# Performance work log

Hardware: AMD Instinct MI355X
Metric: run time of the kernel (lower is better)

Reference implementation:

```python
import jax, jax.numpy as jnp
import numpy as np

N_NODES = 50000
N_EDGES = 600000
D = 128  # input_nf = output_nf = hidden_nf
EDGE_IN = 2 * D + 1   # source, target, radial
NODE_IN = 2 * D       # x, agg


def _glorot(key, shape):
    fan_in, fan_out = shape[0], shape[1]
    lim = float(np.sqrt(6.0 / (fan_in + fan_out)))
    return jax.random.uniform(key, shape, jnp.float32, -lim, lim)


def setup_inputs() -> dict:
    key = jax.random.key(0)
    ks = jax.random.split(key, 16)
    h = jax.random.normal(ks[0], (N_NODES, D), jnp.float32)
    edge_index = jax.random.randint(ks[1], (2, N_EDGES), 0, N_NODES, jnp.int64 if jax.config.read('jax_enable_x64') else jnp.int32)
    coord = jax.random.uniform(ks[2], (N_NODES, 3), jnp.float32)
    l = jnp.array([10.0, 10.0, 10.0], jnp.float32)  # periodic box lengths (non-trainable buffer)
    return {
        'h': h, 'edge_index': edge_index, 'coord': coord, 'num_nodes': N_NODES, 'l': l,
        # edge_mlp: Linear(257,128) SiLU Linear(128,128) SiLU
        'We1': _glorot(ks[3], (EDGE_IN, D)), 'be1': jnp.zeros((D,), jnp.float32),
        'We2': _glorot(ks[4], (D, D)),       'be2': jnp.zeros((D,), jnp.float32),
        # node_mlp: Linear(256,128) SiLU Linear(128,128)
        'Wn1': _glorot(ks[5], (NODE_IN, D)), 'bn1': jnp.zeros((D,), jnp.float32),
        'Wn2': _glorot(ks[6], (D, D)),       'bn2': jnp.zeros((D,), jnp.float32),
        # coord_mlp: Linear(128,128) SiLU Linear(128,1, bias=False, xavier gain=0.001)
        'Wc1': _glorot(ks[7], (D, D)),       'bc1': jnp.zeros((D,), jnp.float32),
        'Wc2': _glorot(ks[8], (D, 1)) * 0.001,
    }


def reference(h, edge_index, coord, num_nodes, l,
              We1, be1, We2, be2, Wn1, bn1, Wn2, bn2, Wc1, bc1, Wc2):
    row, col = edge_index[0], edge_index[1]

    # coord2radial with periodic minimum-image wrap
    diff = coord[row] - coord[col]                       # [E, 3]
    diff = jnp.where(diff > 0.5 * l, diff - l, diff)
    diff = jnp.where(diff < -0.5 * l, diff + l, diff)
    radial = jnp.sum(diff * diff, axis=1, keepdims=True)  # [E, 1]

    # edge model: gather -> concat -> 2-layer SiLU MLP
    eh = jnp.concatenate([h[row], h[col], radial], axis=1)  # [E, 257]
    eh = jax.nn.silu(eh @ We1 + be1)
    edge_feat = jax.nn.silu(eh @ We2 + be2)                 # [E, 128]

    # coord model: trans/agg computed in the original but discarded (dead code);
    # only the periodic remainder of coord is returned.
    coord_out = jnp.remainder(coord, l)

    # node model: scatter-add edge features into nodes, then MLP + residual
    agg = jax.ops.segment_sum(edge_feat, row, num_segments=num_nodes)  # [N, 128]
    nh = jnp.concatenate([h, agg], axis=1)                              # [N, 256]
    nh = jax.nn.silu(nh @ Wn1 + bn1)
    h_out = h + (nh @ Wn2 + bn2)

    return h_out, coord_out, edge_feat
```

## Files before the change

### kernel.cpp

```cpp
#include <hip/hip_runtime.h>
#include <math.h>

#define D 128
#define SXS 264
#define SHS 132
#define SFS 132

typedef unsigned int u32;
typedef unsigned short u16;
typedef __attribute__((ext_vector_type(8))) short bf16x8;
typedef __attribute__((ext_vector_type(4))) float f32x4;
typedef __attribute__((ext_vector_type(2))) float f32x2;

__device__ __forceinline__ float bfl(u32 u) { return __uint_as_float(u << 16); }
__device__ __forceinline__ float bfh(u32 u) { return __uint_as_float(u & 0xFFFF0000u); }
__device__ __forceinline__ u16 f2bf(float f) {
    u32 u = __float_as_uint(f);
    return (u16)((u + 0x7FFFu + ((u >> 16) & 1u)) >> 16);
}
__device__ __forceinline__ u32 cvt_pk_bf16(float lo, float hi) {
    u32 r;
    asm("v_cvt_pk_bf16_f32 %0, %1, %2" : "=v"(r) : "v"(lo), "v"(hi));
    return r;
}
__device__ __forceinline__ u16 cvt1_bf16(float v) { return (u16)cvt_pk_bf16(v, v); }
__device__ __forceinline__ float silu_f(float x) {
    float e = __expf(-x);
    return x * __builtin_amdgcn_rcpf(1.0f + e);
}
__device__ __forceinline__ void atomic_pk_add_bf16(u16* addr, u32 pk) {
    asm volatile("global_atomic_pk_add_bf16 %0, %1, off sc1"
                 :: "v"(addr), "v"(pk) : "memory");
}

__global__ void coord_kernel(const float* __restrict__ coord,
                             const float* __restrict__ lbox,
                             float* __restrict__ out, int n3) {
    int i = blockIdx.x * 256 + threadIdx.x;
    if (i < n3) {
        float ld = lbox[i % 3];
        float c = coord[i];
        float r = fmodf(c, ld);
        if (r < 0.f) r += ld;
        out[i] = r;
    }
}

__global__ void prep_weights(const float* __restrict__ We1, const float* __restrict__ We2,
                             const float* __restrict__ Wn1, const float* __restrict__ Wn2,
                             u16* __restrict__ wt) {
    int i = blockIdx.x * 256 + threadIdx.x;
    if (i < 32768)        { int n = i >> 8, k = i & 255;              wt[i] = f2bf(We1[(size_t)k*D + n]); }
    else if (i < 49152)   { int j = i - 32768; int n = j >> 7, k = j & 127; wt[i] = f2bf(We2[(size_t)k*D + n]); }
    else if (i < 81920)   { int j = i - 49152; int n = j >> 8, k = j & 255; wt[i] = f2bf(Wn1[(size_t)k*D + n]); }
    else if (i < 98304)   { int j = i - 81920; int n = j >> 7, k = j & 127; wt[i] = f2bf(Wn2[(size_t)k*D + n]); }
}

__global__ void hist_kernel(const int* __restrict__ ei, int* __restrict__ cnt, int E) {
    int e = blockIdx.x * 256 + threadIdx.x;
    if (e < E) atomicAdd(&cnt[ei[e]], 1);
}

__global__ void scan1_kernel(const int* __restrict__ cnt, int* __restrict__ offs,
                             int* __restrict__ bsum, int n ) {
    __shared__ int s[256];
    int t = threadIdx.x, b = blockIdx.x;
    int base = b * 1024 + t * 4;
    int v[4];
    #pragma unroll
    for (int i = 0; i < 4; ++i) { int idx = base + i; v[i] = (idx < n - 1) ? cnt[idx] : 0; }
    int lsum = v[0] + v[1] + v[2] + v[3];
    s[t] = lsum; __syncthreads();
    #pragma unroll
    for (int off = 1; off < 256; off <<= 1) {
        int x = (t >= off) ? s[t - off] : 0; __syncthreads();
        s[t] += x; __syncthreads();
    }
    int run = s[t] - lsum;
    #pragma unroll
    for (int i = 0; i < 4; ++i) { int idx = base + i; if (idx < n) offs[idx] = run; run += v[i]; }
    if (t == 255) bsum[b] = s[255];
}

__global__ void scan2_kernel(int* __restrict__ bsum, int nb) {
    __shared__ int s[64];
    int t = threadIdx.x;
    int orig = (t < nb) ? bsum[t] : 0;
    s[t] = orig; __syncthreads();
    #pragma unroll
    for (int off = 1; off < 64; off <<= 1) {
        int x = (t >= off) ? s[t - off] : 0; __syncthreads();
        s[t] += x; __syncthreads();
    }
    if (t < nb) bsum[t] = s[t] - orig;
}

__global__ void scan3_kernel(int* __restrict__ offs, const int* __restrict__ bsum,
                             int* __restrict__ cursor, int n) {
    int i = blockIdx.x * 256 + threadIdx.x;
    if (i < n) {
        int v = offs[i] + bsum[i >> 10];
        offs[i] = v;
        if (i < n - 1) cursor[i] = v;
    }
}

__global__ void scatter_kernel(const int* __restrict__ ei, int* __restrict__ cursor,
                               int* __restrict__ perm, int4* __restrict__ edata, int E) {
    int e = blockIdx.x * 256 + threadIdx.x;
    if (e < E) {
        int r = ei[e];
        int c = ei[(size_t)E + e];
        int p = atomicAdd(&cursor[r], 1);
        if (edata) edata[p] = make_int4(e, r, c, 0);
        else perm[p] = e;
    }
}

__global__ __launch_bounds__(256, 4) void pq_kernel(
    const float* __restrict__ h, const u16* __restrict__ wt,
    const float* __restrict__ be1,
    u16* __restrict__ Pt, u16* __restrict__ Qt,
    int* __restrict__ cursor, int N,
    const float* __restrict__ coord, const float* __restrict__ lbox,
    float* __restrict__ coord_out, int n3, int NBn)
{
    __shared__ __align__(16) u16 sA[64 * SHS];
    __shared__ __align__(16) u16 sO[64 * SHS];

    const int t = threadIdx.x;

    if (blockIdx.x >= NBn) {
        int i = (blockIdx.x - NBn) * 256 + t;
        if (i < n3) {
            float ld = lbox[i % 3];
            float c = coord[i];
            float r = fmodf(c, ld);
            if (r < 0.f) r += ld;
            coord_out[i] = r;
        }
        return;
    }

    const int lane = t & 63;
    const int wid = t >> 6;
    const int n0 = blockIdx.x * 64;

    if (t < 64) { int zi = n0 + t; if (zi < N) cursor[zi] = 0; }

    {
        const int e = t & 63, q = t >> 6;
        int ng = n0 + e; int ns = (ng < N) ? ng : N - 1;
        const float4* src = (const float4*)(h + (size_t)ns * D + q * 32);
        u16* dst = sA + e * SHS + q * 32;
        #pragma unroll
        for (int c = 0; c < 4; ++c) {
            float4 a = src[2 * c], b = src[2 * c + 1];
            *(uint4*)(dst + c * 8) = make_uint4(cvt_pk_bf16(a.x, a.y), cvt_pk_bf16(a.z, a.w),
                                               cvt_pk_bf16(b.x, b.y), cvt_pk_bf16(b.z, b.w));
        }
    }
    __syncthreads();

    const int lrow = lane & 15;
    const int kg = lane >> 4;
    const int g4 = kg * 4;
    const int nbase = wid * 32;

    f32x4 accP[4][2] = {}, accQ[4][2] = {};
    {
        bf16x8 Bt[8], Bm[8];
        #pragma unroll
        for (int nn = 0; nn < 2; ++nn)
            #pragma unroll
            for (int s = 0; s < 4; ++s) {
                const u16* bp = wt + (size_t)(nbase + nn * 16 + lrow) * 256 + s * 32 + kg * 8;
                Bt[nn * 4 + s] = *(const bf16x8*)bp;
                Bm[nn * 4 + s] = *(const bf16x8*)(bp + 128);
            }
        #pragma unroll
        for (int s = 0; s < 4; ++s) {
            bf16x8 a[4];
            #pragma unroll
            for (int m = 0; m < 4; ++m)
                a[m] = *(const bf16x8*)(sA + (m * 16 + lrow) * SHS + s * 32 + kg * 8);
            #pragma unroll
            for (int m = 0; m < 4; ++m)
                #pragma unroll
                for (int nn = 0; nn < 2; ++nn) {
                    accP[m][nn] = __builtin_amdgcn_mfma_f32_16x16x32_bf16(a[m], Bt[nn * 4 + s], accP[m][nn], 0, 0, 0);
                    accQ[m][nn] = __builtin_amdgcn_mfma_f32_16x16x32_bf16(a[m], Bm[nn * 4 + s], accQ[m][nn], 0, 0, 0);
                }
        }
    }

    #pragma unroll
    for (int nn = 0; nn < 2; ++nn) {
        int outc = nbase + nn * 16 + lrow;
        float bb = be1[outc];
        #pragma unroll
        for (int m = 0; m < 4; ++m)
            #pragma unroll
            for (int r = 0; r < 4; ++r)
                sO[(m * 16 + g4 + r) * SHS + outc] = cvt1_bf16(accP[m][nn][r] + bb);
    }
    __syncthreads();
    {
        const int f4 = t & 15, rb = t >> 4;
        #pragma unroll
        for (int p = 0; p < 4; ++p) {
            int row = rb + p * 16;
            int ng = n0 + row;
            if (ng < N)
                *(uint4*)(Pt + (size_t)ng * D + f4 * 8) = *(const uint4*)(sO + row * SHS + f4 * 8);
        }
    }
    __syncthreads();
    #pragma unroll
    for (int nn = 0; nn < 2; ++nn) {
        int outc = nbase + nn * 16 + lrow;
        #pragma unroll
        for (int m = 0; m < 4; ++m)
            #pragma unroll
            for (int r = 0; r < 4; ++r)
                sO[(m * 16 + g4 + r) * SHS + outc] = cvt1_bf16(accQ[m][nn][r]);
    }
    __syncthreads();
    {
        const int f4 = t & 15, rb = t >> 4;
        #pragma unroll
        for (int p = 0; p < 4; ++p) {
            int row = rb + p * 16;
            int ng = n0 + row;
            if (ng < N)
                *(uint4*)(Qt + (size_t)ng * D + f4 * 8) = *(const uint4*)(sO + row * SHS + f4 * 8);
        }
    }
}

__global__ __launch_bounds__(256, 8) void edge_pq_kernel(
    const u16* __restrict__ Pt, const u16* __restrict__ Qt,
    const int* __restrict__ ei, const int* __restrict__ perm,
    const int4* __restrict__ edata,
    const float* __restrict__ coord, const float* __restrict__ lbox,
    const u16* __restrict__ wt, const float* __restrict__ We1,
    const float* __restrict__ be2,
    float* __restrict__ ef_out, float* __restrict__ aggf,
    u16* __restrict__ agg16, int E)
{
    __shared__ __align__(16) u16 uni[64 * SHS];
    __shared__ int srow[64], scol[64], sEid[64];
    __shared__ float sRad[64];
    __shared__ float sW[128];
    u16* sH1 = uni;
    u16* sE16 = uni;

    const int t = threadIdx.x;
    const int lane = t & 63;
    const int wid = t >> 6;

    int p0;
    {
        const int nwg = gridDim.x;
        const int orig = blockIdx.x;
        const int q = nwg >> 3, r = nwg & 7;
        const int xcd = orig & 7, idx = orig >> 3;
        const int tile = (xcd < r ? xcd * (q + 1) : r * (q + 1) + (xcd - r) * q) + idx;
        p0 = tile * 64;
    }

    if (t < 64) {
        int slot = p0 + t;
        bool valid = slot < E;
        int cs = valid ? slot : (E - 1);
        int eg, rr, cc;
        if (edata) {
            int4 ed = edata[cs];
            eg = ed.x; rr = ed.y; cc = ed.z;
        } else {
            eg = perm[cs];
            rr = ei[eg];
            cc = ei[(size_t)E + eg];
        }
        sEid[t] = valid ? eg : -1;
        srow[t] = rr;
        scol[t] = cc;
        float rad = 0.f;
        #pragma unroll
        for (int d3 = 0; d3 < 3; ++d3) {
            float df = coord[(size_t)rr * 3 + d3] - coord[(size_t)cc * 3 + d3];
            float ld = lbox[d3];
            df = (df >  0.5f * ld) ? df - ld : df;
            df = (df < -0.5f * ld) ? df + ld : df;
            rad += df * df;
        }
        sRad[t] = rad;
    } else if (t < 192) {
        sW[t - 64] = We1[(size_t)256 * D + (t - 64)];
    }
    __syncthreads();

    {
        const int e = t & 63, q = t >> 6;
        const u16* Pp = Pt + (size_t)srow[e] * D;
        const u16* Qp = Qt + (size_t)scol[e] * D;
        const float rad = sRad[e];
        #pragma unroll
        for (int c0 = 0; c0 < 4; ++c0) {
            int j0 = q * 32 + c0 * 8;
            uint4 pu = *(const uint4*)(Pp + j0);
            uint4 qu = *(const uint4*)(Qp + j0);
            u32 pa[4] = {pu.x, pu.y, pu.z, pu.w};
            u32 qa[4] = {qu.x, qu.y, qu.z, qu.w};
            u32 ow[4];
            #pragma unroll
            for (int k = 0; k < 4; ++k) {
                float w0 = sW[j0 + 2 * k], w1 = sW[j0 + 2 * k + 1];
                float v0 = silu_f(bfl(pa[k]) + bfl(qa[k]) + rad * w0);
                float v1 = silu_f(bfh(pa[k]) + bfh(qa[k]) + rad * w1);
                ow[k] = cvt_pk_bf16(v0, v1);
            }
            *(uint4*)(sH1 + e * SHS + j0) = make_uint4(ow[0], ow[1], ow[2], ow[3]);
        }
    }
    __syncthreads();

    const int lrow = lane & 15;
    const int kg = lane >> 4;
    const int g4 = kg * 4;
    const int nbase = wid * 32;

    f32x4 acc2[4][2] = {};
    {
        bf16x8 B2[8];
        #pragma unroll
        for (int nn = 0; nn < 2; ++nn)
            #pragma unroll
            for (int s = 0; s < 4; ++s)
                B2[nn * 4 + s] = *(const bf16x8*)(wt + 32768 + (size_t)(nbase + nn * 16 + lrow) * 128 + s * 32 + kg * 8);
        #pragma unroll
        for (int s = 0; s < 4; ++s) {
            bf16x8 a[4];
            #pragma unroll
            for (int m = 0; m < 4; ++m)
                a[m] = *(const bf16x8*)(sH1 + (m * 16 + lrow) * SHS + s * 32 + kg * 8);
            #pragma unroll
            for (int m = 0; m < 4; ++m)
                #pragma unroll
                for (int nn = 0; nn < 2; ++nn)
                    acc2[m][nn] = __builtin_amdgcn_mfma_f32_16x16x32_bf16(a[m], B2[nn * 4 + s], acc2[m][nn], 0, 0, 0);
        }
    }
    __syncthreads();

    #pragma unroll
    for (int nn = 0; nn < 2; ++nn) {
        int outc = nbase + nn * 16 + lrow;
        float bb = be2[outc];
        #pragma unroll
        for (int m = 0; m < 4; ++m)
            #pragma unroll
            for (int r = 0; r < 4; ++r)
                sE16[(m * 16 + g4 + r) * SHS + outc] = cvt1_bf16(silu_f(acc2[m][nn][r] + bb));
    }
    __syncthreads();

    if (agg16) {
        const int cp = t & 63;
        const int g = t >> 6;
        const int ebeg = g * 16, eend = ebeg + 16;
        float r0 = 0.f, r1 = 0.f;
        int prev = srow[ebeg];
        for (int e = ebeg; e < eend; ++e) {
            int r = srow[e];
            if (r != prev) {
                if (r0 != 0.f || r1 != 0.f)
                    atomic_pk_add_bf16(agg16 + (size_t)prev * D + 2 * cp, cvt_pk_bf16(r0, r1));
                r0 = 0.f; r1 = 0.f; prev = r;
            }
            int eg = sEid[e];
            if (eg >= 0) {
                u32 pk2 = *(const u32*)(sE16 + e * SHS + 2 * cp);
                float v0 = bfl(pk2), v1 = bfh(pk2);
                f32x2 vv = {v0, v1};
                __builtin_nontemporal_store(vv, (f32x2*)&ef_out[(size_t)eg * D + 2 * cp]);
                r0 += v0; r1 += v1;
            }
        }
        if (r0 != 0.f || r1 != 0.f)
            atomic_pk_add_bf16(agg16 + (size_t)prev * D + 2 * cp, cvt_pk_bf16(r0, r1));
    } else {
        const int ct = t & 127;
        const int half = t >> 7;
        const int ebeg = half * 32, eend = ebeg + 32;
        float run = 0.f;
        int prev = srow[ebeg];
        for (int e = ebeg; e < eend; ++e) {
            int r = srow[e];
            if (r != prev) {
                if (run != 0.f) atomicAdd(&aggf[(size_t)prev * D + ct], run);
                run = 0.f; prev = r;
            }
            int eg = sEid[e];
            if (eg >= 0) {
                float v = __uint_as_float((u32)sE16[e * SHS + ct] << 16);
                __builtin_nontemporal_store(v, &ef_out[(size_t)eg * D + ct]);
                run += v;
            }
        }
        if (run != 0.f) atomicAdd(&aggf[(size_t)prev * D + ct], run);
    }
}

__global__ __launch_bounds__(256, 3) void edge_fb_kernel(
    const float* __restrict__ h,
    const int* __restrict__ ei, const int* __restrict__ perm,
    const float* __restrict__ coord, const float* __restrict__ lbox,
    const u16* __restrict__ wt,
    const float* __restrict__ We1, const float* __restrict__ be1,
    const float* __restrict__ be2,
    float* __restrict__ ef_out, float* __restrict__ aggf, int E)
{
    __shared__ __align__(16) u16 sX[64 * SXS];
    __shared__ __align__(16) u16 sH1[64 * SHS];
    __shared__ int srow[64], scol[64], sEid[64];
    __shared__ float sRad[64];

    const int t = threadIdx.x;
    const int lane = t & 63;
    const int wid = t >> 6;

    int p0;
    {
        const int nwg = gridDim.x;
        const int orig = blockIdx.x;
        const int q = nwg >> 3, r = nwg & 7;
        const int xcd = orig & 7, idx = orig >> 3;
        const int tile = (xcd < r ? xcd * (q + 1) : r * (q + 1) + (xcd - r) * q) + idx;
        p0 = tile * 64;
    }

    if (t < 64) {
        int slot = p0 + t;
        int eg = perm[(slot < E) ? slot : (E - 1)];
        sEid[t] = (p0 + t < E) ? eg : -1;
        srow[t] = ei[eg];
        scol[t] = ei[(size_t)E + eg];
    }
    __syncthreads();

    {
        const int e = t & 63;
        const int q = t >> 6;
        const int r = srow[e], c = scol[e];
        const float4* src = (const float4*)((q < 2) ? (h + (size_t)r * D + (q & 1) * 64)
                                                    : (h + (size_t)c * D + (q & 1) * 64));
        u16* dst = sX + e * SXS + q * 64;
        #pragma unroll
        for (int i = 0; i < 8; ++i) {
            float4 a = src[2 * i], b = src[2 * i + 1];
            *(uint4*)(dst + i * 8) = make_uint4(cvt_pk_bf16(a.x, a.y), cvt_pk_bf16(a.z, a.w),
                                               cvt_pk_bf16(b.x, b.y), cvt_pk_bf16(b.z, b.w));
        }
        if (t < 64) {
            int rr = srow[t], cc = scol[t];
            float rad = 0.f;
            #pragma unroll
            for (int d3 = 0; d3 < 3; ++d3) {
                float df = coord[(size_t)rr * 3 + d3] - coord[(size_t)cc * 3 + d3];
                float ld = lbox[d3];
                df = (df >  0.5f * ld) ? df - ld : df;
                df = (df < -0.5f * ld) ? df + ld : df;
                rad += df * df;
            }
            sRad[t] = rad;
        }
    }
    __syncthreads();

    const int lrow = lane & 15;
    const int kg = lane >> 4;
    const int g4 = kg * 4;
    const int nbase = wid * 32;

    f32x4 acc[4][2] = {};
    {
        bf16x8 B1[16];
        #pragma unroll
        for (int nn = 0; nn < 2; ++nn)
            #pragma unroll
            for (int s = 0; s < 8; ++s)
                B1[nn * 8 + s] = *(const bf16x8*)(wt + (size_t)(nbase + nn * 16 + lrow) * 256 + s * 32 + kg * 8);
        #pragma unroll
        for (int s = 0; s < 8; ++s) {
            bf16x8 a[4];
            #pragma unroll
            for (int m = 0; m < 4; ++m)
                a[m] = *(const bf16x8*)(sX + (m * 16 + lrow) * SXS + s * 32 + kg * 8);
            #pragma unroll
            for (int m = 0; m < 4; ++m)
                #pragma unroll
                for (int nn = 0; nn < 2; ++nn)
                    acc[m][nn] = __builtin_amdgcn_mfma_f32_16x16x32_bf16(a[m], B1[nn * 8 + s], acc[m][nn], 0, 0, 0);
        }
    }

    #pragma unroll
    for (int nn = 0; nn < 2; ++nn) {
        int outc = nbase + nn * 16 + lrow;
        float wl = We1[(size_t)256 * D + outc];
        float bb = be1[outc];
        #pragma unroll
        for (int m = 0; m < 4; ++m)
            #pragma unroll
            for (int r = 0; r < 4; ++r) {
                int e = m * 16 + g4 + r;
                float v = acc[m][nn][r] + sRad[e] * wl + bb;
                sH1[e * SHS + outc] = cvt1_bf16(silu_f(v));
            }
    }
    __syncthreads();

    f32x4 acc2[4][2] = {};
    {
        bf16x8 B2[8];
        #pragma unroll
        for (int nn = 0; nn < 2; ++nn)
            #pragma unroll
            for (int s = 0; s < 4; ++s)
                B2[nn * 4 + s] = *(const bf16x8*)(wt + 32768 + (size_t)(nbase + nn * 16 + lrow) * 128 + s * 32 + kg * 8);
        #pragma unroll
        for (int s = 0; s < 4; ++s) {
            bf16x8 a[4];
            #pragma unroll
            for (int m = 0; m < 4; ++m)
                a[m] = *(const bf16x8*)(sH1 + (m * 16 + lrow) * SHS + s * 32 + kg * 8);
            #pragma unroll
            for (int m = 0; m < 4; ++m)
                #pragma unroll
                for (int nn = 0; nn < 2; ++nn)
                    acc2[m][nn] = __builtin_amdgcn_mfma_f32_16x16x32_bf16(a[m], B2[nn * 4 + s], acc2[m][nn], 0, 0, 0);
        }
    }
    __syncthreads();

    float* sXf = (float*)sX;
    #pragma unroll
    for (int nn = 0; nn < 2; ++nn) {
        int outc = nbase + nn * 16 + lrow;
        float bb = be2[outc];
        #pragma unroll
        for (int m = 0; m < 4; ++m)
            #pragma unroll
            for (int r = 0; r < 4; ++r)
                sXf[(m * 16 + g4 + r) * SFS + outc] = silu_f(acc2[m][nn][r] + bb);
    }
    __syncthreads();

    {
        const int ct = t & 127;
        const int half = t >> 7;
        const int ebeg = half * 32, eend = ebeg + 32;
        float run = 0.f;
        int prev = srow[ebeg];
        for (int e = ebeg; e < eend; ++e) {
            int r = srow[e];
            if (r != prev) {
                if (run != 0.f) atomicAdd(&aggf[(size_t)prev * D + ct], run);
                run = 0.f; prev = r;
            }
            int eg = sEid[e];
            if (eg >= 0) {
                float v = sXf[e * SFS + ct];
                __builtin_nontemporal_store(v, &ef_out[(size_t)eg * D + ct]);
                run += v;
            }
        }
        if (run != 0.f) atomicAdd(&aggf[(size_t)prev * D + ct], run);
    }
}

__global__ __launch_bounds__(256, 4) void node_kernel(
    const float* __restrict__ h, const float* __restrict__ aggf,
    const u16* __restrict__ agg16,
    const u16* __restrict__ wt,
    const float* __restrict__ bn1, const float* __restrict__ bn2,
    float* __restrict__ h_out, int N)
{
    __shared__ __align__(16) u16 uni[64 * SXS];
    u16* sX = uni;
    u16* sH1 = uni;
    float* sXf = (float*)uni;

    const int t = threadIdx.x;
    const int lane = t & 63;
    const int wid = t >> 6;
    const int n0 = blockIdx.x * 64;

    {
        const int e = t & 63;
        const int q = t >> 6;
        int ng = n0 + e; int ns = (ng < N) ? ng : N - 1;
        u16* dst = sX + e * SXS + q * 64;
        if (q >= 2 && agg16) {
            const u16* src = agg16 + (size_t)ns * D + (q & 1) * 64;
            #pragma unroll
            for (int i = 0; i < 8; ++i)
                *(uint4*)(dst + i * 8) = *(const uint4*)(src + i * 8);
        } else {
            const float4* src = (const float4*)(((q < 2) ? h : aggf) + (size_t)ns * D + (q & 1) * 64);
            #pragma unroll
            for (int i = 0; i < 8; ++i) {
                float4 a = src[2 * i], b = src[2 * i + 1];
                *(uint4*)(dst + i * 8) = make_uint4(cvt_pk_bf16(a.x, a.y), cvt_pk_bf16(a.z, a.w),
                                                   cvt_pk_bf16(b.x, b.y), cvt_pk_bf16(b.z, b.w));
            }
        }
    }
    __syncthreads();

    const int lrow = lane & 15;
    const int kg = lane >> 4;
    const int g4 = kg * 4;
    const int nbase = wid * 32;

    f32x4 acc[4][2] = {};
    {
        bf16x8 B1[16];
        #pragma unroll
        for (int nn = 0; nn < 2; ++nn)
            #pragma unroll
            for (int s = 0; s < 8; ++s)
                B1[nn * 8 + s] = *(const bf16x8*)(wt + 49152 + (size_t)(nbase + nn * 16 + lrow) * 256 + s * 32 + kg * 8);
        #pragma unroll
        for (int s = 0; s < 8; ++s) {
            bf16x8 a[4];
            #pragma unroll
            for (int m = 0; m < 4; ++m)
                a[m] = *(const bf16x8*)(sX + (m * 16 + lrow) * SXS + s * 32 + kg * 8);
            #pragma unroll
            for (int m = 0; m < 4; ++m)
                #pragma unroll
                for (int nn = 0; nn < 2; ++nn)
                    acc[m][nn] = __builtin_amdgcn_mfma_f32_16x16x32_bf16(a[m], B1[nn * 8 + s], acc[m][nn], 0, 0, 0);
        }
    }
    __syncthreads();

    #pragma unroll
    for (int nn = 0; nn < 2; ++nn) {
        int outc = nbase + nn * 16 + lrow;
        float bb = bn1[outc];
        #pragma unroll
        for (int m = 0; m < 4; ++m)
            #pragma unroll
            for (int r = 0; r < 4; ++r)
                sH1[(m * 16 + g4 + r) * SHS + outc] = cvt1_bf16(silu_f(acc[m][nn][r] + bb));
    }
    __syncthreads();

    f32x4 acc2[4][2] = {};
    {
        bf16x8 B2[8];
        #pragma unroll
        for (int nn = 0; nn < 2; ++nn)
            #pragma unroll
            for (int s = 0; s < 4; ++s)
                B2[nn * 4 + s] = *(const bf16x8*)(wt + 81920 + (size_t)(nbase + nn * 16 + lrow) * 128 + s * 32 + kg * 8);
        #pragma unroll
        for (int s = 0; s < 4; ++s) {
            bf16x8 a[4];
            #pragma unroll
            for (int m = 0; m < 4; ++m)
                a[m] = *(const bf16x8*)(sH1 + (m * 16 + lrow) * SHS + s * 32 + kg * 8);
            #pragma unroll
            for (int m = 0; m < 4; ++m)
                #pragma unroll
                for (int nn = 0; nn < 2; ++nn)
                    acc2[m][nn] = __builtin_amdgcn_mfma_f32_16x16x32_bf16(a[m], B2[nn * 4 + s], acc2[m][nn], 0, 0, 0);
        }
    }
    __syncthreads();

    #pragma unroll
    for (int nn = 0; nn < 2; ++nn) {
        int outc = nbase + nn * 16 + lrow;
        float bb = bn2[outc];
        #pragma unroll
        for (int m = 0; m < 4; ++m)
            #pragma unroll
            for (int r = 0; r < 4; ++r)
                sXf[(m * 16 + g4 + r) * SFS + outc] = acc2[m][nn][r] + bb;
    }
    __syncthreads();

    {
        const int f4 = t & 31;
        const int nb = t >> 5;
        #pragma unroll
        for (int i = 0; i < 8; ++i) {
            int nl = nb + i * 8;
            int ng = n0 + nl;
            if (ng < N) {
                f32x4 v = *(const f32x4*)&sXf[nl * SFS + f4 * 4];
                const f32x4 hv = *(const f32x4*)&h[(size_t)ng * D + f4 * 4];
                v += hv;
                __builtin_nontemporal_store(v, (f32x4*)&h_out[(size_t)ng * D + f4 * 4]);
            }
        }
    }
}

extern "C" void kernel_launch(void* const* d_in, const int* in_sizes, int n_in,
                              void* d_out, int out_size, void* d_ws, size_t ws_size,
                              hipStream_t stream) {
    const float* h     = (const float*)d_in[0];
    const int*   ei    = (const int*)d_in[1];
    const float* coord = (const float*)d_in[2];
    const float* lbox  = (const float*)d_in[4];
    const float* We1   = (const float*)d_in[5];
    const float* be1   = (const float*)d_in[6];
    const float* We2   = (const float*)d_in[7];
    const float* be2   = (const float*)d_in[8];
    const float* Wn1   = (const float*)d_in[9];
    const float* bn1   = (const float*)d_in[10];
    const float* Wn2   = (const float*)d_in[11];
    const float* bn2   = (const float*)d_in[12];

    const int N = in_sizes[0] / D;
    const int E = in_sizes[1] / 2;

    float* out       = (float*)d_out;
    float* h_out     = out;
    float* coord_out = out + (size_t)N * D;
    float* ef_out    = coord_out + (size_t)N * 3;
    float* aggf      = h_out;

    int* wsi = (int*)d_ws;
    u16* wt     = (u16*)d_ws;
    int* offs   = wsi + 49152;
    int* cursor = offs + (N + 8);
    int* bsum   = cursor + (N + 8);
    int* perm   = bsum + 64;
    u16* Pt     = (u16*)(perm + E);
    u16* Qt     = Pt + (size_t)N * D;
    int4* edata = (int4*)(((uintptr_t)(Qt + (size_t)N * D) + 15) & ~(uintptr_t)15);
    u16* agg16  = (u16*)(edata + E);

    size_t need_pq  = (size_t)((char*)(Qt + (size_t)N * D) - (char*)d_ws);
    size_t need_ed  = (size_t)((char*)(edata + E) - (char*)d_ws);
    size_t need_a16 = (size_t)((char*)(agg16 + (size_t)N * D) - (char*)d_ws);
    const bool use_pq  = ws_size >= need_pq;
    const bool use_ed  = use_pq && ws_size >= need_ed;
    const bool use_a16 = use_ed && ws_size >= need_a16;
    int4* edp  = use_ed ? edata : nullptr;
    u16*  a16p = use_a16 ? agg16 : nullptr;

    const int nb1 = (N + 1 + 1023) / 1024;

    prep_weights<<<384, 256, 0, stream>>>(We1, We2, Wn1, Wn2, wt);
    if (use_pq) {
        const int NBn = (N + 63) / 64;
        const int NBc = (N * 3 + 255) / 256;
        pq_kernel<<<NBn + NBc, 256, 0, stream>>>(h, wt, be1, Pt, Qt, cursor, N,
                                                 coord, lbox, coord_out, N * 3, NBn);
    } else {
        hipMemsetAsync(cursor, 0, (size_t)N * sizeof(int), stream);
        coord_kernel<<<(N * 3 + 255) / 256, 256, 0, stream>>>(coord, lbox, coord_out, N * 3);
    }

    if (use_a16)
        hipMemsetAsync(agg16, 0, (size_t)N * D * sizeof(u16), stream);
    else
        hipMemsetAsync(aggf, 0, (size_t)N * D * sizeof(float), stream);

    hist_kernel<<<(E + 255) / 256, 256, 0, stream>>>(ei, cursor, E);
    scan1_kernel<<<nb1, 256, 0, stream>>>(cursor, offs, bsum, N + 1);
    scan2_kernel<<<1, 64, 0, stream>>>(bsum, nb1);
    scan3_kernel<<<(N + 1 + 255) / 256, 256, 0, stream>>>(offs, bsum, cursor, N + 1);
    scatter_kernel<<<(E + 255) / 256, 256, 0, stream>>>(ei, cursor, perm, edp, E);

    if (use_pq)
        edge_pq_kernel<<<(E + 63) / 64, 256, 0, stream>>>(
            Pt, Qt, ei, perm, edp, coord, lbox, wt, We1, be2, ef_out, aggf, a16p, E);
    else
        edge_fb_kernel<<<(E + 63) / 64, 256, 0, stream>>>(
            h, ei, perm, coord, lbox, wt, We1, be1, be2, ef_out, aggf, E);

    node_kernel<<<(N + 63) / 64, 256, 0, stream>>>(
        h, aggf, a16p, wt, bn1, bn2, h_out, N);
}
```

Before: 243.9 us.

## Merge setup launches, use single-pass decoupled scan, vectorize hist/scatter

```diff
diff --git a/kernel.cpp b/kernel.cpp
--- a/kernel.cpp
+++ b/kernel.cpp
@@ -46,23 +46,87 @@
     }
 }
 
-__global__ void prep_weights(const float* __restrict__ We1, const float* __restrict__ We2,
-                             const float* __restrict__ Wn1, const float* __restrict__ Wn2,
-                             u16* __restrict__ wt) {
-    int i = blockIdx.x * 256 + threadIdx.x;
-    if (i < 32768)        { int n = i >> 8, k = i & 255;              wt[i] = f2bf(We1[(size_t)k*D + n]); }
-    else if (i < 49152)   { int j = i - 32768; int n = j >> 7, k = j & 127; wt[i] = f2bf(We2[(size_t)k*D + n]); }
-    else if (i < 81920)   { int j = i - 49152; int n = j >> 8, k = j & 255; wt[i] = f2bf(Wn1[(size_t)k*D + n]); }
-    else if (i < 98304)   { int j = i - 81920; int n = j >> 7, k = j & 127; wt[i] = f2bf(Wn2[(size_t)k*D + n]); }
-}
-
-__global__ void hist_kernel(const int* __restrict__ ei, int* __restrict__ cnt, int E) {
-    int e = blockIdx.x * 256 + threadIdx.x;
-    if (e < E) atomicAdd(&cnt[ei[e]], 1);
+__global__ __launch_bounds__(256) void prep_plus_kernel(
+    const float* __restrict__ We1, const float* __restrict__ We2,
+    const float* __restrict__ Wn1, const float* __restrict__ Wn2,
+    u16* __restrict__ wt,
+    int* __restrict__ cursor, int N,
+    u16* __restrict__ agg16, long agg_n,
+    int* __restrict__ bstate,
+    int B1, int B2, int B3)
+{
+    const int b = blockIdx.x, t = threadIdx.x;
+    if (b < B1) {
+        int i = b * 256 + t;
+        if (i < 32768)        { int n = i >> 8, k = i & 255;              wt[i] = f2bf(We1[(size_t)k*D + n]); }
+        else if (i < 49152)   { int j = i - 32768; int n = j >> 7, k = j & 127; wt[i] = f2bf(We2[(size_t)k*D + n]); }
+        else if (i < 81920)   { int j = i - 49152; int n = j >> 8, k = j & 255; wt[i] = f2bf(Wn1[(size_t)k*D + n]); }
+        else                  { int j = i - 81920; int n = j >> 7, k = j & 127; wt[i] = f2bf(Wn2[(size_t)k*D + n]); }
+    } else if (b < B2) {
+        int i = ((b - B1) * 256 + t) * 4;
+        if (i + 3 < N) *(int4*)(cursor + i) = make_int4(0, 0, 0, 0);
+        else for (int k = 0; k < 4; ++k) if (i + k < N) cursor[i + k] = 0;
+    } else if (b < B3) {
+        long i = ((long)(b - B2) * 256 + t) * 8;
+        if (agg16 && i < agg_n) *(uint4*)(agg16 + i) = make_uint4(0, 0, 0, 0);
+    } else {
+        if (t < 64) bstate[t] = 0;
+    }
+}
+
+__global__ void hist4_kernel(const int* __restrict__ ei, int* __restrict__ cnt, int E) {
+    int i = (blockIdx.x * 256 + threadIdx.x) * 4;
+    if (i + 3 < E) {
+        int4 r = *(const int4*)(ei + i);
+        atomicAdd(&cnt[r.x], 1); atomicAdd(&cnt[r.y], 1);
+        atomicAdd(&cnt[r.z], 1); atomicAdd(&cnt[r.w], 1);
+    } else {
+        for (int k = 0; k < 4; ++k) if (i + k < E) atomicAdd(&cnt[ei[i + k]], 1);
+    }
+}
+
+__global__ __launch_bounds__(256) void scan_lb_kernel(int* __restrict__ cursor,
+                                                      int* __restrict__ bstate, int n) {
+    __shared__ int s[256];
+    __shared__ int sExcl;
+    const int t = threadIdx.x, b = blockIdx.x;
+    const int base = b * 1024 + t * 4;
+    int v[4];
+    #pragma unroll
+    for (int i = 0; i < 4; ++i) { int idx = base + i; v[i] = (idx < n - 1) ? cursor[idx] : 0; }
+    int lsum = v[0] + v[1] + v[2] + v[3];
+    s[t] = lsum; __syncthreads();
+    #pragma unroll
+    for (int off = 1; off < 256; off <<= 1) {
+        int x = (t >= off) ? s[t - off] : 0; __syncthreads();
+        s[t] += x; __syncthreads();
+    }
+    if (t == 0)
+        __hip_atomic_store(&bstate[b], 0x40000000 | s[255], __ATOMIC_RELEASE, __HIP_MEMORY_SCOPE_AGENT);
+    if (t < 64) {
+        int val = 0;
+        if (t < b) {
+            int st;
+            do { st = __hip_atomic_load(&bstate[t], __ATOMIC_ACQUIRE, __HIP_MEMORY_SCOPE_AGENT); }
+            while (!(st & 0x40000000));
+            val = st & 0x3FFFFFFF;
+        }
+        #pragma unroll
+        for (int off = 1; off < 64; off <<= 1) val += __shfl_xor(val, off, 64);
+        if (t == 0) sExcl = val;
+    }
+    __syncthreads();
+    int run = sExcl + s[t] - lsum;
+    #pragma unroll
+    for (int i = 0; i < 4; ++i) {
+        int idx = base + i;
+        if (idx < n - 1) cursor[idx] = run;
+        run += v[i];
+    }
 }
 
 __global__ void scan1_kernel(const int* __restrict__ cnt, int* __restrict__ offs,
-                             int* __restrict__ bsum, int n ) {
+                             int* __restrict__ bsum, int n) {
     __shared__ int s[256];
     int t = threadIdx.x, b = blockIdx.x;
     int base = b * 1024 + t * 4;
@@ -105,23 +169,41 @@
     }
 }
 
-__global__ void scatter_kernel(const int* __restrict__ ei, int* __restrict__ cursor,
-                               int* __restrict__ perm, int4* __restrict__ edata, int E) {
-    int e = blockIdx.x * 256 + threadIdx.x;
-    if (e < E) {
-        int r = ei[e];
-        int c = ei[(size_t)E + e];
-        int p = atomicAdd(&cursor[r], 1);
-        if (edata) edata[p] = make_int4(e, r, c, 0);
-        else perm[p] = e;
+__global__ void scatter4_kernel(const int* __restrict__ ei, int* __restrict__ cursor,
+                                int* __restrict__ perm, int4* __restrict__ edata, int E) {
+    int i = (blockIdx.x * 256 + threadIdx.x) * 4;
+    if (i + 3 < E) {
+        int4 r = *(const int4*)(ei + i);
+        int4 c = *(const int4*)(ei + (size_t)E + i);
+        int p0 = atomicAdd(&cursor[r.x], 1);
+        int p1 = atomicAdd(&cursor[r.y], 1);
+        int p2 = atomicAdd(&cursor[r.z], 1);
+        int p3 = atomicAdd(&cursor[r.w], 1);
+        if (edata) {
+            edata[p0] = make_int4(i,     r.x, c.x, 0);
+            edata[p1] = make_int4(i + 1, r.y, c.y, 0);
+            edata[p2] = make_int4(i + 2, r.z, c.z, 0);
+            edata[p3] = make_int4(i + 3, r.w, c.w, 0);
+        } else {
+            perm[p0] = i; perm[p1] = i + 1; perm[p2] = i + 2; perm[p3] = i + 3;
+        }
+    } else {
+        for (int k = 0; k < 4; ++k) {
+            int e = i + k;
+            if (e < E) {
+                int r = ei[e], c = ei[(size_t)E + e];
+                int p = atomicAdd(&cursor[r], 1);
+                if (edata) edata[p] = make_int4(e, r, c, 0);
+                else perm[p] = e;
+            }
+        }
     }
 }
 
 __global__ __launch_bounds__(256, 4) void pq_kernel(
     const float* __restrict__ h, const u16* __restrict__ wt,
     const float* __restrict__ be1,
-    u16* __restrict__ Pt, u16* __restrict__ Qt,
-    int* __restrict__ cursor, int N,
+    u16* __restrict__ Pt, u16* __restrict__ Qt, int N,
     const float* __restrict__ coord, const float* __restrict__ lbox,
     float* __restrict__ coord_out, int n3, int NBn)
 {
@@ -145,8 +227,6 @@
     const int lane = t & 63;
     const int wid = t >> 6;
     const int n0 = blockIdx.x * 64;
-
-    if (t < 64) { int zi = n0 + t; if (zi < N) cursor[zi] = 0; }
 
     {
         const int e = t & 63, q = t >> 6;
@@ -757,28 +837,37 @@
     u16*  a16p = use_a16 ? agg16 : nullptr;
 
     const int nb1 = (N + 1 + 1023) / 1024;
-
-    prep_weights<<<384, 256, 0, stream>>>(We1, We2, Wn1, Wn2, wt);
+    const bool lbscan = nb1 <= 64;
+
+    const long agg_n = (long)N * D;
+    const int B1 = 384;
+    const int B2 = B1 + (N / 4 + 255) / 256;
+    const int B3 = B2 + (use_a16 ? (int)((agg_n / 8 + 255) / 256) : 0);
+    const int Bt = B3 + 1;
+    prep_plus_kernel<<<Bt, 256, 0, stream>>>(We1, We2, Wn1, Wn2, wt,
+                                             cursor, N, a16p, agg_n, bsum, B1, B2, B3);
+
     if (use_pq) {
         const int NBn = (N + 63) / 64;
         const int NBc = (N * 3 + 255) / 256;
-        pq_kernel<<<NBn + NBc, 256, 0, stream>>>(h, wt, be1, Pt, Qt, cursor, N,
+        pq_kernel<<<NBn + NBc, 256, 0, stream>>>(h, wt, be1, Pt, Qt, N,
                                                  coord, lbox, coord_out, N * 3, NBn);
     } else {
-        hipMemsetAsync(cursor, 0, (size_t)N * sizeof(int), stream);
         coord_kernel<<<(N * 3 + 255) / 256, 256, 0, stream>>>(coord, lbox, coord_out, N * 3);
     }
 
-    if (use_a16)
-        hipMemsetAsync(agg16, 0, (size_t)N * D * sizeof(u16), stream);
-    else
+    if (!use_a16)
         hipMemsetAsync(aggf, 0, (size_t)N * D * sizeof(float), stream);
 
-    hist_kernel<<<(E + 255) / 256, 256, 0, stream>>>(ei, cursor, E);
-    scan1_kernel<<<nb1, 256, 0, stream>>>(cursor, offs, bsum, N + 1);
-    scan2_kernel<<<1, 64, 0, stream>>>(bsum, nb1);
-    scan3_kernel<<<(N + 1 + 255) / 256, 256, 0, stream>>>(offs, bsum, cursor, N + 1);
-    scatter_kernel<<<(E + 255) / 256, 256, 0, stream>>>(ei, cursor, perm, edp, E);
+    hist4_kernel<<<(E / 4 + 255) / 256, 256, 0, stream>>>(ei, cursor, E);
+    if (lbscan) {
+        scan_lb_kernel<<<nb1, 256, 0, stream>>>(cursor, bsum, N + 1);
+    } else {
+        scan1_kernel<<<nb1, 256, 0, stream>>>(cursor, offs, bsum, N + 1);
+        scan2_kernel<<<1, 64, 0, stream>>>(bsum, nb1);
+        scan3_kernel<<<(N + 1 + 255) / 256, 256, 0, stream>>>(offs, bsum, cursor, N + 1);
+    }
+    scatter4_kernel<<<(E / 4 + 255) / 256, 256, 0, stream>>>(ei, cursor, perm, edp, E);
 
     if (use_pq)
         edge_pq_kernel<<<(E + 63) / 64, 256, 0, stream>>>(
```

Result: no change. 241.8 us (median of 2 runs) (-0.9%).
